# Optimization experiments

Measured on AMD Instinct MI355X. Metric: run time of the kernel, lower is better.

## Reference

```python
import jax, jax.numpy as jnp
import numpy as np

N_QUBITS = 4
N_LAYERS = 6
BATCH = 524288
C64 = jnp.complex64


def setup_inputs() -> dict:
    key = jax.random.key(0)
    k1, k2, k3 = jax.random.split(key, 3)
    x = jax.random.normal(k1, (BATCH, N_QUBITS), dtype=jnp.float32)
    weights = jax.random.normal(k2, (N_LAYERS, N_QUBITS, 3), dtype=jnp.float32)
    bias = jax.random.normal(k3, (3,), dtype=jnp.float32)
    class_bias = jnp.zeros((1,), dtype=jnp.float32)
    return {"x": x, "weights": weights, "bias": bias, "class_bias": class_bias}


def _rx(t):
    # RX(t) = [[cos(t/2), -i sin(t/2)], [-i sin(t/2), cos(t/2)]]
    c = jnp.cos(0.5 * t)
    s = jnp.sin(0.5 * t)
    return jnp.stack([jnp.stack([c + 0j, -1j * s]), jnp.stack([-1j * s, c + 0j])]).astype(C64)


def _ry(t):
    # RY(t) = [[cos, -sin], [sin, cos]] (real)
    c = jnp.cos(0.5 * t)
    s = jnp.sin(0.5 * t)
    return jnp.stack([jnp.stack([c, -s]), jnp.stack([s, c])]).astype(C64)


def _rz(t):
    # RZ(t) = diag(exp(-i t/2), exp(+i t/2))
    e = jnp.exp(-0.5j * t).astype(C64)
    return jnp.diag(jnp.stack([e, jnp.conj(e)]))


def _apply_1q(psi, U, q):
    # psi: [B,2,2,2,2]; contract 2x2 U into qubit axis (1+q)
    ax = 1 + q
    out = jnp.tensordot(U, psi, axes=([1], [ax]))  # [2, B, ...]
    return jnp.moveaxis(out, 0, ax)


def _cnot(psi, ctrl, tgt):
    ax_c, ax_t = 1 + ctrl, 1 + tgt
    a0 = jax.lax.index_in_dim(psi, 0, ax_c, keepdims=True)
    a1 = jnp.flip(jax.lax.index_in_dim(psi, 1, ax_c, keepdims=True), axis=ax_t)
    return jnp.concatenate([a0, a1], axis=ax_c)


def _circuit(x, weights):
    # AngleEmbedding (RX rotations) on |0000>: per-qubit amps [cos(x/2), -i sin(x/2)]
    half = 0.5 * x
    c = jnp.cos(half)
    s = jnp.sin(half)
    a = jnp.stack([c.astype(C64), (-1j * s).astype(C64)], axis=-1)  # [B, nq, 2]
    psi = jnp.einsum('bi,bj,bk,bl->bijkl', a[:, 0], a[:, 1], a[:, 2], a[:, 3])
    for layer in range(N_LAYERS):
        for cw, tw in ((0, 1), (1, 2), (2, 3), (3, 0)):
            psi = _cnot(psi, cw, tw)
        for q in range(N_QUBITS):
            psi = _apply_1q(psi, _rx(weights[layer, q, 0]), q)
            psi = _apply_1q(psi, _ry(weights[layer, q, 1]), q)
            psi = _apply_1q(psi, _rz(weights[layer, q, 2]), q)
    p = psi.real ** 2 + psi.imag ** 2  # probabilities [B,2,2,2,2]
    z = jnp.array([1.0, -1.0], dtype=jnp.float32)
    evs = jnp.stack([
        jnp.einsum('bijkl,i->b', p, z),
        jnp.einsum('bijkl,j->b', p, z),
        jnp.einsum('bijkl,k->b', p, z),
        jnp.einsum('bijkl,l->b', p, z),
    ], axis=-1)  # [B, 4], matches torch.stack(res).permute(1,0)
    return evs


def reference(x, weights, bias, class_bias):
    # bias / class_bias are parameters of the original module but are never
    # used inside the quantum circuit; output depends only on x and weights.
    return _circuit(x, weights)
```

## Files before the change

kernel.cpp:

```cpp
#include <hip/hip_runtime.h>
#include <math.h>

#define NQ 4
#define NL 6
#define BATCH 524288
#define EPT 4
#define LP 17

struct C2 { float re, im; };

__device__ __forceinline__ C2 cmul(C2 a, C2 b) {
    return C2{ __builtin_fmaf(a.re, b.re, -a.im * b.im),
               __builtin_fmaf(a.re, b.im,  a.im * b.re) };
}

__global__ __launch_bounds__(256) void qone_kernel(const float4* __restrict__ x,
                                                   const float* __restrict__ w,
                                                   float4* __restrict__ out) {
    __shared__ float  sU[NL * NQ * 8];
    __shared__ float2 sL[NL][16 * LP];
    __shared__ float2 sP[3][16 * LP];
    __shared__ float2 sD[16 * LP];
    __shared__ float4 sV4[128];

    const int tid = threadIdx.x;
    const int base = blockIdx.x * (256 * EPT) + tid;

    float m[EPT][16];
#pragma unroll
    for (int e = 0; e < EPT; ++e) {
        const float4 xv = x[base + e * 256];
        float c0, s0, c1, s1, c2, s2, c3, s3;
        __sincosf(0.5f * xv.x, &s0, &c0);
        __sincosf(0.5f * xv.y, &s1, &c1);
        __sincosf(0.5f * xv.z, &s2, &c2);
        __sincosf(0.5f * xv.w, &s3, &c3);
        float ab[4];
        ab[0] = c0 * c1; ab[1] = c0 * s1; ab[2] = s0 * c1; ab[3] = s0 * s1;
        float abc[8];
#pragma unroll
        for (int k = 0; k < 4; ++k) { abc[2 * k] = ab[k] * c2; abc[2 * k + 1] = ab[k] * s2; }
#pragma unroll
        for (int k = 0; k < 8; ++k) { m[e][2 * k] = abc[k] * c3; m[e][2 * k + 1] = abc[k] * s3; }
    }

    if (tid < NL * NQ) {
        const float a = w[tid * 3 + 0];
        const float b = w[tid * 3 + 1];
        const float g = w[tid * 3 + 2];
        float ca, sa, cb, sb, cg, sg;
        sincosf(0.5f * a, &sa, &ca);
        sincosf(0.5f * b, &sb, &cb);
        sincosf(0.5f * g, &sg, &cg);
        C2 M00{cb * ca,  sb * sa};
        C2 M01{-sb * ca, -cb * sa};
        C2 M10{sb * ca,  -cb * sa};
        C2 M11{cb * ca,  -sb * sa};
        C2 em{cg, -sg}, ep{cg, sg};
        C2 U00 = cmul(em, M00), U01 = cmul(em, M01);
        C2 U10 = cmul(ep, M10), U11 = cmul(ep, M11);
        float* o = &sU[tid * 8];
        o[0] = U00.re; o[1] = U00.im; o[2] = U01.re; o[3] = U01.im;
        o[4] = U10.re; o[5] = U10.im; o[6] = U11.re; o[7] = U11.im;
    }
    __syncthreads();

    const int r = tid >> 4;
    const int c = tid & 15;

    {
        int b0 = (c >> 3) & 1, b1 = (c >> 2) & 1, b2 = (c >> 1) & 1, b3 = c & 1;
        b1 ^= b0; b2 ^= b1; b3 ^= b2; b0 ^= b3;
        const int r0 = (r >> 3) & 1, r1 = (r >> 2) & 1, r2 = (r >> 1) & 1, r3 = r & 1;
        const int o0 = (r0 * 2 + b0) * 2;
        const int o1 = (r1 * 2 + b1) * 2;
        const int o2 = (r2 * 2 + b2) * 2;
        const int o3 = (r3 * 2 + b3) * 2;
#pragma unroll
        for (int l = 0; l < NL; ++l) {
            const float* g = &sU[l * 32];
            C2 a{g[o0], g[o0 + 1]};
            a = cmul(a, C2{g[8  + o1], g[8  + o1 + 1]});
            a = cmul(a, C2{g[16 + o2], g[16 + o2 + 1]});
            a = cmul(a, C2{g[24 + o3], g[24 + o3 + 1]});
            sL[l][r * LP + c] = make_float2(a.re, a.im);
        }
    }
    __syncthreads();

#pragma unroll
    for (int s = 0; s < 3; ++s) {
        float re = 0.f, im = 0.f;
#pragma unroll
        for (int k = 0; k < 16; ++k) {
            const float2 xk = sL[2 * s + 1][r * LP + k];
            const float2 yk = sL[2 * s][k * LP + c];
            re = __builtin_fmaf(xk.x, yk.x, re); re = __builtin_fmaf(-xk.y, yk.y, re);
            im = __builtin_fmaf(xk.x, yk.y, im); im = __builtin_fmaf( xk.y, yk.x, im);
        }
        sP[s][r * LP + c] = make_float2(re, im);
    }
    __syncthreads();

    {
        float re = 0.f, im = 0.f;
#pragma unroll
        for (int k = 0; k < 16; ++k) {
            const float2 xk = sP[1][r * LP + k];
            const float2 yk = sP[0][k * LP + c];
            re = __builtin_fmaf(xk.x, yk.x, re); re = __builtin_fmaf(-xk.y, yk.y, re);
            im = __builtin_fmaf(xk.x, yk.y, im); im = __builtin_fmaf( xk.y, yk.x, im);
        }
        sD[r * LP + c] = make_float2(re, im);
    }
    __syncthreads();

    {
        float re = 0.f, im = 0.f;
#pragma unroll
        for (int k = 0; k < 16; ++k) {
            const float2 xk = sP[2][r * LP + k];
            const float2 yk = sD[k * LP + c];
            re = __builtin_fmaf(xk.x, yk.x, re); re = __builtin_fmaf(-xk.y, yk.y, re);
            im = __builtin_fmaf(xk.x, yk.y, im); im = __builtin_fmaf( xk.y, yk.x, im);
        }
        const int p4 = __popc(c) & 3;
        float wr, wi;
        if      (p4 == 0) { wr = re;  wi = im;  }
        else if (p4 == 1) { wr = im;  wi = -re; }
        else if (p4 == 2) { wr = -re; wi = -im; }
        else              { wr = -im; wi = re;  }
        float* sVf = reinterpret_cast<float*>(sV4);
        reinterpret_cast<float2*>(&sVf[r * 32 + 2 * c])[0] = make_float2(wr, wi);
    }
    __syncthreads();

    float ev[EPT][4];
#pragma unroll
    for (int e = 0; e < EPT; ++e)
#pragma unroll
        for (int q = 0; q < 4; ++q) ev[e][q] = 0.f;

#pragma unroll
    for (int rr = 0; rr < 16; ++rr) {
        float4 row[8];
#pragma unroll
        for (int k = 0; k < 8; ++k) row[k] = sV4[rr * 8 + k];
#pragma unroll
        for (int e = 0; e < EPT; ++e) {
            float re = 0.f, im = 0.f;
#pragma unroll
            for (int k = 0; k < 8; ++k) {
                re = __builtin_fmaf(m[e][2 * k],     row[k].x, re);
                im = __builtin_fmaf(m[e][2 * k],     row[k].y, im);
                re = __builtin_fmaf(m[e][2 * k + 1], row[k].z, re);
                im = __builtin_fmaf(m[e][2 * k + 1], row[k].w, im);
            }
            const float p = __builtin_fmaf(re, re, im * im);
            if (rr & 8) ev[e][0] -= p; else ev[e][0] += p;
            if (rr & 4) ev[e][1] -= p; else ev[e][1] += p;
            if (rr & 2) ev[e][2] -= p; else ev[e][2] += p;
            if (rr & 1) ev[e][3] -= p; else ev[e][3] += p;
        }
    }

#pragma unroll
    for (int e = 0; e < EPT; ++e) {
        out[base + e * 256] = make_float4(ev[e][0], ev[e][1], ev[e][2], ev[e][3]);
    }
}

extern "C" void kernel_launch(void* const* d_in, const int* in_sizes, int n_in,
                              void* d_out, int out_size, void* d_ws, size_t ws_size,
                              hipStream_t stream) {
    const float4* x = (const float4*)d_in[0];
    const float*  w = (const float*)d_in[1];
    float4* out = (float4*)d_out;

    const int blocks = BATCH / (256 * EPT);
    qone_kernel<<<blocks, 256, 0, stream>>>(x, w, out);
}
```

Baseline: 19.21 us.

## Split output rows across waves with scalar-broadcast unitary and LDS reduction

Restructures the final amplitude stage so each of 8 waves owns two rows of the 16x16 circuit unitary. The wave broadcasts those rows into uniform registers via readfirstlane, and each lane processes one sample per pass over 16 passes. Per-wave partial expectation values are double-buffered in shared memory, and one rotating wave reduces and writes them. This removes the per-sample full 16-row matvec and the LDS row reads of the old layout. In exchange it adds a block-wide barrier on every pass and leaves half the threads idle during unitary construction.

```diff
diff --git a/kernel.cpp b/kernel.cpp
--- a/kernel.cpp
+++ b/kernel.cpp
@@ -4,8 +4,9 @@
 #define NQ 4
 #define NL 6
 #define BATCH 524288
-#define EPT 4
 #define LP 17
+#define NPASS 16
+#define NBLK (BATCH / (64 * NPASS))
 
 struct C2 { float re, im; };
 
@@ -14,35 +15,23 @@
                __builtin_fmaf(a.re, b.im,  a.im * b.re) };
 }
 
-__global__ __launch_bounds__(256) void qone_kernel(const float4* __restrict__ x,
-                                                   const float* __restrict__ w,
-                                                   float4* __restrict__ out) {
+__device__ __forceinline__ float rfl(float v) {
+    return __uint_as_float(__builtin_amdgcn_readfirstlane(__float_as_uint(v)));
+}
+
+__global__ __launch_bounds__(512) void qsg_kernel(const float4* __restrict__ x,
+                                                  const float* __restrict__ w,
+                                                  float4* __restrict__ out) {
     __shared__ float  sU[NL * NQ * 8];
     __shared__ float2 sL[NL][16 * LP];
     __shared__ float2 sP[3][16 * LP];
-    __shared__ float2 sD[16 * LP];
-    __shared__ float4 sV4[128];
+    __shared__ float2 sDm[16 * LP];
+    __shared__ float  sVf[16 * 32];
+    __shared__ float4 sEv[2][8 * 64];
 
-    const int tid = threadIdx.x;
-    const int base = blockIdx.x * (256 * EPT) + tid;
-
-    float m[EPT][16];
-#pragma unroll
-    for (int e = 0; e < EPT; ++e) {
-        const float4 xv = x[base + e * 256];
-        float c0, s0, c1, s1, c2, s2, c3, s3;
-        __sincosf(0.5f * xv.x, &s0, &c0);
-        __sincosf(0.5f * xv.y, &s1, &c1);
-        __sincosf(0.5f * xv.z, &s2, &c2);
-        __sincosf(0.5f * xv.w, &s3, &c3);
-        float ab[4];
-        ab[0] = c0 * c1; ab[1] = c0 * s1; ab[2] = s0 * c1; ab[3] = s0 * s1;
-        float abc[8];
-#pragma unroll
-        for (int k = 0; k < 4; ++k) { abc[2 * k] = ab[k] * c2; abc[2 * k + 1] = ab[k] * s2; }
-#pragma unroll
-        for (int k = 0; k < 8; ++k) { m[e][2 * k] = abc[k] * c3; m[e][2 * k + 1] = abc[k] * s3; }
-    }
+    const int tid  = threadIdx.x;
+    const int lane = tid & 63;
+    const int wv   = tid >> 6;
 
     if (tid < NL * NQ) {
         const float a = w[tid * 3 + 0];
@@ -65,10 +54,8 @@
     }
     __syncthreads();
 
-    const int r = tid >> 4;
-    const int c = tid & 15;
-
-    {
+    if (tid < 256) {
+        const int r = tid >> 4, c = tid & 15;
         int b0 = (c >> 3) & 1, b1 = (c >> 2) & 1, b2 = (c >> 1) & 1, b3 = c & 1;
         b1 ^= b0; b2 ^= b1; b3 ^= b2; b0 ^= b3;
         const int r0 = (r >> 3) & 1, r1 = (r >> 2) & 1, r2 = (r >> 1) & 1, r3 = r & 1;
@@ -88,21 +75,24 @@
     }
     __syncthreads();
 
+    if (tid < 256) {
+        const int r = tid >> 4, c = tid & 15;
 #pragma unroll
-    for (int s = 0; s < 3; ++s) {
-        float re = 0.f, im = 0.f;
+        for (int s = 0; s < 3; ++s) {
+            float re = 0.f, im = 0.f;
 #pragma unroll
-        for (int k = 0; k < 16; ++k) {
-            const float2 xk = sL[2 * s + 1][r * LP + k];
-            const float2 yk = sL[2 * s][k * LP + c];
-            re = __builtin_fmaf(xk.x, yk.x, re); re = __builtin_fmaf(-xk.y, yk.y, re);
-            im = __builtin_fmaf(xk.x, yk.y, im); im = __builtin_fmaf( xk.y, yk.x, im);
+            for (int k = 0; k < 16; ++k) {
+                const float2 xk = sL[2 * s + 1][r * LP + k];
+                const float2 yk = sL[2 * s][k * LP + c];
+                re = __builtin_fmaf(xk.x, yk.x, re); re = __builtin_fmaf(-xk.y, yk.y, re);
+                im = __builtin_fmaf(xk.x, yk.y, im); im = __builtin_fmaf( xk.y, yk.x, im);
+            }
+            sP[s][r * LP + c] = make_float2(re, im);
         }
-        sP[s][r * LP + c] = make_float2(re, im);
     }
     __syncthreads();
-
-    {
+    if (tid < 256) {
+        const int r = tid >> 4, c = tid & 15;
         float re = 0.f, im = 0.f;
 #pragma unroll
         for (int k = 0; k < 16; ++k) {
@@ -111,16 +101,16 @@
             re = __builtin_fmaf(xk.x, yk.x, re); re = __builtin_fmaf(-xk.y, yk.y, re);
             im = __builtin_fmaf(xk.x, yk.y, im); im = __builtin_fmaf( xk.y, yk.x, im);
         }
-        sD[r * LP + c] = make_float2(re, im);
+        sDm[r * LP + c] = make_float2(re, im);
     }
     __syncthreads();
-
-    {
+    if (tid < 256) {
+        const int r = tid >> 4, c = tid & 15;
         float re = 0.f, im = 0.f;
 #pragma unroll
         for (int k = 0; k < 16; ++k) {
             const float2 xk = sP[2][r * LP + k];
-            const float2 yk = sD[k * LP + c];
+            const float2 yk = sDm[k * LP + c];
             re = __builtin_fmaf(xk.x, yk.x, re); re = __builtin_fmaf(-xk.y, yk.y, re);
             im = __builtin_fmaf(xk.x, yk.y, im); im = __builtin_fmaf( xk.y, yk.x, im);
         }
@@ -130,43 +120,69 @@
         else if (p4 == 1) { wr = im;  wi = -re; }
         else if (p4 == 2) { wr = -re; wi = -im; }
         else              { wr = -im; wi = re;  }
-        float* sVf = reinterpret_cast<float*>(sV4);
-        reinterpret_cast<float2*>(&sVf[r * 32 + 2 * c])[0] = make_float2(wr, wi);
+        sVf[r * 32 + 2 * c]     = wr;
+        sVf[r * 32 + 2 * c + 1] = wi;
     }
     __syncthreads();
 
-    float ev[EPT][4];
+    const int row0 = 2 * wv, row1 = 2 * wv + 1;
+    float uRe0[16], uIm0[16], uRe1[16], uIm1[16];
 #pragma unroll
-    for (int e = 0; e < EPT; ++e)
+    for (int c = 0; c < 16; ++c) {
+        const float2 v0 = *reinterpret_cast<const float2*>(&sVf[row0 * 32 + 2 * c]);
+        const float2 v1 = *reinterpret_cast<const float2*>(&sVf[row1 * 32 + 2 * c]);
+        uRe0[c] = rfl(v0.x); uIm0[c] = rfl(v0.y);
+        uRe1[c] = rfl(v1.x); uIm1[c] = rfl(v1.y);
+    }
+    const float sg0 = (wv & 4) ? -1.f : 1.f;
+    const float sg1 = (wv & 2) ? -1.f : 1.f;
+    const float sg2 = (wv & 1) ? -1.f : 1.f;
+
+    const int gbase = blockIdx.x * (64 * NPASS);
+
+    for (int p = 0; p <= NPASS; ++p) {
+        if (p < NPASS) {
+            const float4 xv = x[gbase + p * 64 + lane];
+            float c0, s0, c1, s1, c2, s2, c3, s3;
+            __sincosf(0.5f * xv.x, &s0, &c0);
+            __sincosf(0.5f * xv.y, &s1, &c1);
+            __sincosf(0.5f * xv.z, &s2, &c2);
+            __sincosf(0.5f * xv.w, &s3, &c3);
+            float m[16];
+            {
+                float ab[4];
+                ab[0] = c0 * c1; ab[1] = c0 * s1; ab[2] = s0 * c1; ab[3] = s0 * s1;
+                float abc[8];
 #pragma unroll
-        for (int q = 0; q < 4; ++q) ev[e][q] = 0.f;
-
+                for (int k = 0; k < 4; ++k) { abc[2 * k] = ab[k] * c2; abc[2 * k + 1] = ab[k] * s2; }
 #pragma unroll
-    for (int rr = 0; rr < 16; ++rr) {
-        float4 row[8];
+                for (int k = 0; k < 8; ++k) { m[2 * k] = abc[k] * c3; m[2 * k + 1] = abc[k] * s3; }
+            }
+            float re0 = 0.f, im0 = 0.f, re1 = 0.f, im1 = 0.f;
 #pragma unroll
-        for (int k = 0; k < 8; ++k) row[k] = sV4[rr * 8 + k];
+            for (int c = 0; c < 16; ++c) {
+                re0 = __builtin_fmaf(m[c], uRe0[c], re0);
+                im0 = __builtin_fmaf(m[c], uIm0[c], im0);
+                re1 = __builtin_fmaf(m[c], uRe1[c], re1);
+                im1 = __builtin_fmaf(m[c], uIm1[c], im1);
+            }
+            const float p0 = __builtin_fmaf(re0, re0, im0 * im0);
+            const float p1 = __builtin_fmaf(re1, re1, im1 * im1);
+            const float S = p0 + p1;
+            const float D = p0 - p1;
+            sEv[p & 1][wv * 64 + lane] = make_float4(sg0 * S, sg1 * S, sg2 * S, D);
+        }
+        if (p > 0 && wv == ((p - 1) & 7)) {
+            const int b = (p - 1) & 1;
+            float4 a = sEv[b][lane];
 #pragma unroll
-        for (int e = 0; e < EPT; ++e) {
-            float re = 0.f, im = 0.f;
-#pragma unroll
-            for (int k = 0; k < 8; ++k) {
-                re = __builtin_fmaf(m[e][2 * k],     row[k].x, re);
-                im = __builtin_fmaf(m[e][2 * k],     row[k].y, im);
-                re = __builtin_fmaf(m[e][2 * k + 1], row[k].z, re);
-                im = __builtin_fmaf(m[e][2 * k + 1], row[k].w, im);
+            for (int ww = 1; ww < 8; ++ww) {
+                const float4 t = sEv[b][ww * 64 + lane];
+                a.x += t.x; a.y += t.y; a.z += t.z; a.w += t.w;
             }
-            const float p = __builtin_fmaf(re, re, im * im);
-            if (rr & 8) ev[e][0] -= p; else ev[e][0] += p;
-            if (rr & 4) ev[e][1] -= p; else ev[e][1] += p;
-            if (rr & 2) ev[e][2] -= p; else ev[e][2] += p;
-            if (rr & 1) ev[e][3] -= p; else ev[e][3] += p;
+            out[gbase + (p - 1) * 64 + lane] = a;
         }
-    }
-
-#pragma unroll
-    for (int e = 0; e < EPT; ++e) {
-        out[base + e * 256] = make_float4(ev[e][0], ev[e][1], ev[e][2], ev[e][3]);
+        __syncthreads();
     }
 }
 
@@ -177,6 +193,5 @@
     const float*  w = (const float*)d_in[1];
     float4* out = (float4*)d_out;
 
-    const int blocks = BATCH / (256 * EPT);
-    qone_kernel<<<blocks, 256, 0, stream>>>(x, w, out);
+    qsg_kernel<<<NBLK, 512, 0, stream>>>(x, w, out);
 }
```

Result: slower. 27.97 us (+45.6%).
